# Performance work log

Hardware: AMD Instinct MI355X
Metric: run time of the kernel (lower is better)

Reference implementation:

```python
import jax, jax.numpy as jnp
import numpy as np

# Dimensions (LRA BigBird base-ish config)
B, S, D = 4, 4096, 512
H, DH = 8, 64          # num_heads, head_dim = qkv_dim // num_heads
M = 2048               # mlp_dim
BS = 64                # block_size
NB = S // BS           # number of blocks = 64
R = 3                  # num random blocks per row (BigBird default)
K = 8                  # max gathered key blocks per row: 3 window + 2 global + 3 random
SEED = 0               # connectivity_seed
LN_EPS = 1e-6


def _block_indices():
    """Static BigBird connectivity for interior query blocks (rows 1..NB-2).

    Each interior block attends to: window {i-1,i,i+1}, globals {0, NB-1},
    and R random blocks (seeded, disjoint from window/global). Rows where
    window overlaps globals have fewer unique blocks and are padded+masked.
    """
    rng = np.random.RandomState(SEED)
    idx = np.zeros((NB - 2, K), np.int32)
    msk = np.zeros((NB - 2, K), bool)
    for row, i in enumerate(range(1, NB - 1)):
        fixed = sorted({0, NB - 1, i - 1, i, i + 1})
        allowed = [b for b in range(NB) if b not in fixed]
        rand = rng.choice(allowed, size=R, replace=False).tolist()
        blocks = fixed + rand
        idx[row, :len(blocks)] = blocks
        msk[row, :len(blocks)] = True
    return jnp.asarray(idx), jnp.asarray(msk)

IDX, KMASK = _block_indices()  # [NB-2, K] int32 / bool
NEG = -1e9


def _ln(x, scale, bias):
    mu = jnp.mean(x, axis=-1, keepdims=True)
    var = jnp.mean(jnp.square(x - mu), axis=-1, keepdims=True)
    return (x - mu) * jax.lax.rsqrt(var + LN_EPS) * scale + bias


def setup_inputs() -> dict:
    key = jax.random.key(0)
    ks = jax.random.split(key, 7)

    def xav(k, shape, fan_in, fan_out):
        lim = float(np.sqrt(6.0 / (fan_in + fan_out)))
        return jax.random.uniform(k, shape, jnp.float32, -lim, lim)

    return {
        "inputs": jax.random.normal(ks[0], (B, S, D), jnp.float32),
        "ln1_scale": jnp.ones((D,), jnp.float32),
        "ln1_bias": jnp.zeros((D,), jnp.float32),
        "wq": xav(ks[1], (D, H, DH), D, DH),
        "wk": xav(ks[2], (D, H, DH), D, DH),
        "wv": xav(ks[3], (D, H, DH), D, DH),
        "wo": xav(ks[4], (H, DH, D), D, D),
        "ln2_scale": jnp.ones((D,), jnp.float32),
        "ln2_bias": jnp.zeros((D,), jnp.float32),
        "w1": xav(ks[5], (D, M), D, M),
        "b1": jnp.zeros((M,), jnp.float32),
        "w2": xav(ks[6], (M, D), M, D),
        "b2": jnp.zeros((D,), jnp.float32),
    }


def reference(inputs, ln1_scale, ln1_bias, wq, wk, wv, wo,
              ln2_scale, ln2_bias, w1, b1, w2, b2):
    x = _ln(inputs, ln1_scale, ln1_bias)
    scale = 1.0 / jnp.sqrt(jnp.asarray(DH, x.dtype))
    q = jnp.einsum("bsd,dhk->bshk", x, wq) * scale
    k = jnp.einsum("bsd,dhk->bshk", x, wk)
    v = jnp.einsum("bsd,dhk->bshk", x, wv)

    # block layout: [B, H, NB, BS, DH]
    qb = q.reshape(B, NB, BS, H, DH).transpose(0, 3, 1, 2, 4)
    kb = k.reshape(B, NB, BS, H, DH).transpose(0, 3, 1, 2, 4)
    vb = v.reshape(B, NB, BS, H, DH).transpose(0, 3, 1, 2, 4)

    # ---- interior query blocks: sparse (window + global + random) keys ----
    q_int = qb[:, :, 1:NB - 1]                       # [B,H,NB-2,BS,DH]
    k_sel = kb[:, :, IDX]                            # [B,H,NB-2,K,BS,DH]
    v_sel = vb[:, :, IDX]
    s = jnp.einsum("bhnqd,bhnkjd->bhnqkj", q_int, k_sel)
    s = jnp.where(KMASK[None, None, :, None, :, None], s, NEG)
    p = jax.nn.softmax(s.reshape(B, H, NB - 2, BS, K * BS), axis=-1)
    p = p.reshape(B, H, NB - 2, BS, K, BS)
    o_int = jnp.einsum("bhnqkj,bhnkjd->bhnqd", p, v_sel)

    # ---- global query blocks (first & last): full attention ----
    q_g = qb[:, :, jnp.array([0, NB - 1])]           # [B,H,2,BS,DH]
    kf = k.transpose(0, 2, 1, 3)                     # [B,H,S,DH]
    vf = v.transpose(0, 2, 1, 3)
    sg = jnp.einsum("bhgqd,bhtd->bhgqt", q_g, kf)
    pg = jax.nn.softmax(sg, axis=-1)
    o_g = jnp.einsum("bhgqt,bhtd->bhgqd", pg, vf)

    o = jnp.concatenate([o_g[:, :, :1], o_int, o_g[:, :, 1:]], axis=2)
    o = o.transpose(0, 2, 3, 1, 4).reshape(B, S, H, DH)
    attn = jnp.einsum("bshd,hde->bse", o, wo)        # output proj, no bias

    x = attn + inputs                                 # residual 1
    y = _ln(x, ln2_scale, ln2_bias)
    y = jax.nn.gelu(jnp.einsum("bsd,dm->bsm", y, w1) + b1)
    y = jnp.einsum("bsm,md->bsd", y, w2) + b2
    return x + y                                      # residual 2
```

## Files before the change

kernel.cpp:

```cpp
#include <hip/hip_runtime.h>
#include <cstdint>
#include <cstddef>

typedef __bf16 bf16;
typedef __bf16 bf16x8 __attribute__((ext_vector_type(8)));
typedef float  f32x4  __attribute__((ext_vector_type(4)));

#define DEVINL static __device__ __forceinline__

DEVINL void gl2lds16(const void* g, void* l) {
  __builtin_amdgcn_global_load_lds((__attribute__((address_space(1))) void*)g,
                                   (__attribute__((address_space(3))) void*)l,
                                   16, 0, 0);
}

DEVINL float loadf(const void* p, size_t i, int isf) {
  return isf ? ((const float*)p)[i] : (float)((const bf16*)p)[i];
}

struct TabArg { unsigned char idx[62][8]; unsigned char cnt[62]; };

struct HostMT {
  unsigned mt[624]; int mti;
  void seed(unsigned s) {
    mt[0] = s;
    for (int i = 1; i < 624; ++i) mt[i] = 1812433253u * (mt[i-1] ^ (mt[i-1] >> 30)) + (unsigned)i;
    mti = 624;
  }
  unsigned next() {
    if (mti == 624) {
      for (int i = 0; i < 624; ++i) {
        unsigned y = (mt[i] & 0x80000000u) | (mt[(i+1)%624] & 0x7fffffffu);
        unsigned v = mt[(i+397)%624] ^ (y >> 1);
        if (y & 1u) v ^= 0x9908b0dfu;
        mt[i] = v;
      }
      mti = 0;
    }
    unsigned y = mt[mti++];
    y ^= y >> 11; y ^= (y << 7) & 0x9d2c5680u; y ^= (y << 15) & 0xefc60000u; y ^= y >> 18;
    return y;
  }
  unsigned interval(unsigned mx) {
    if (mx == 0) return 0;
    unsigned mask = mx;
    mask |= mask>>1; mask |= mask>>2; mask |= mask>>4; mask |= mask>>8; mask |= mask>>16;
    unsigned v = next() & mask;
    while (v > mx) v = next() & mask;
    return v;
  }
};

static void build_tab(TabArg* t) {
  HostMT rng; rng.seed(0u);
  for (int row = 0; row < 62; ++row) {
    int i = row + 1;
    bool fix[64] = {};
    fix[0] = true; fix[63] = true; fix[i-1] = true; fix[i] = true; fix[i+1] = true;
    int fixed[5]; int nf = 0; int allowed[64]; int na = 0;
    for (int b = 0; b < 64; ++b) { if (fix[b]) fixed[nf++] = b; else allowed[na++] = b; }
    int perm[64];
    for (int j = 0; j < na; ++j) perm[j] = j;
    for (int j = na - 1; j > 0; --j) {
      unsigned kk = rng.interval((unsigned)j);
      int tmp = perm[j]; perm[j] = perm[kk]; perm[kk] = tmp;
    }
    int nb = 0;
    for (int j = 0; j < nf; ++j) t->idx[row][nb++] = (unsigned char)fixed[j];
    for (int j = 0; j < 3;  ++j) t->idx[row][nb++] = (unsigned char)allowed[perm[j]];
    t->cnt[row] = (unsigned char)nb;
    for (int j = nb; j < 8; ++j) t->idx[row][j] = 0;
  }
}

__global__ __launch_bounds__(256) void detect_kernel(const unsigned short* __restrict__ x,
                                                     int* __restrict__ flag) {
  __shared__ int cnt[256];
  int c = 0;
  for (int i = threadIdx.x; i < 8192; i += 256) {
    int e = (x[i] >> 7) & 0xFF;
    if (e >= 0xC6) c++;
  }
  cnt[threadIdx.x] = c;
  __syncthreads();
  for (int s = 128; s > 0; s >>= 1) {
    if (threadIdx.x < s) cnt[threadIdx.x] += cnt[threadIdx.x + s];
    __syncthreads();
  }
  if (threadIdx.x == 0) *flag = (cnt[0] > 32) ? 1 : 0;
}

struct P6 { const void* s[6]; bf16* d[6]; int n[6]; };
__global__ __launch_bounds__(256) void cvt6_kernel(const int* __restrict__ flagp, P6 p) {
  int isf = *flagp;
  int which = blockIdx.x;
  const void* src = p.s[which];
  bf16* dst = p.d[which];
  int n = p.n[which];
  int i8 = threadIdx.x * 8;
  if (i8 >= n) return;
  bf16x8 o;
  if (isf) {
    const float* s = (const float*)src + i8;
    f32x4 a = *(const f32x4*)s;
    f32x4 b = *(const f32x4*)(s + 4);
#pragma unroll
    for (int j = 0; j < 4; ++j) { o[j] = (bf16)a[j]; o[4+j] = (bf16)b[j]; }
  } else {
    o = *(const bf16x8*)((const bf16*)src + i8);
  }
  *(bf16x8*)(dst + i8) = o;
}

__global__ __launch_bounds__(256) void transpose_any_kernel(const int* __restrict__ flagp,
                                                            const void* __restrict__ in,
                                                            bf16* __restrict__ out, int R, int C) {
  __shared__ __align__(16) bf16 sT[64 * 72];
  int isf = *flagp;
  int cb = C >> 6;
  int br = blockIdx.x / cb, bc = blockIdx.x % cb;
  int r0 = br * 64, c0 = bc * 64;
  int t = threadIdx.x;
#pragma unroll
  for (int p = 0; p < 2; ++p) {
    int cid = p * 256 + t;
    int r = cid >> 3, c = cid & 7;
    bf16x8 v;
    if (isf) {
      const float* s = (const float*)in + (size_t)(r0 + r) * C + c0 + c * 8;
      f32x4 a = *(const f32x4*)s;
      f32x4 b = *(const f32x4*)(s + 4);
#pragma unroll
      for (int j = 0; j < 4; ++j) { v[j] = (bf16)a[j]; v[4+j] = (bf16)b[j]; }
    } else {
      v = *(const bf16x8*)((const bf16*)in + (size_t)(r0 + r) * C + c0 + c * 8);
    }
    *(bf16x8*)&sT[r * 72 + c * 8] = v;
  }
  __syncthreads();
#pragma unroll
  for (int p = 0; p < 2; ++p) {
    int cid = p * 256 + t;
    int oc = cid >> 3, rc = cid & 7;
    bf16x8 vv;
#pragma unroll
    for (int i = 0; i < 8; ++i) vv[i] = sT[(rc * 8 + i) * 72 + oc];
    *(bf16x8*)&out[(size_t)(c0 + oc) * R + r0 + rc * 8] = vv;
  }
}

__global__ __launch_bounds__(256) void ln_any_kernel(const int* __restrict__ flagp,
                                                     const void* __restrict__ x,
                                                     const bf16* __restrict__ sc,
                                                     const bf16* __restrict__ bi,
                                                     bf16* __restrict__ out) {
  int isf = *flagp;
  int row  = blockIdx.x * 4 + (threadIdx.x >> 6);
  int lane = threadIdx.x & 63;
  float f[8];
  if (isf) {
    const float* xf = (const float*)x + (size_t)row * 512 + lane * 8;
    f32x4 a = *(const f32x4*)xf;
    f32x4 b = *(const f32x4*)(xf + 4);
#pragma unroll
    for (int j = 0; j < 4; ++j) { f[j] = a[j]; f[4+j] = b[j]; }
  } else {
    bf16x8 v = ((const bf16x8*)((const bf16*)x + (size_t)row * 512))[lane];
#pragma unroll
    for (int j = 0; j < 8; ++j) f[j] = (float)v[j];
  }
  float s = 0.f, s2 = 0.f;
#pragma unroll
  for (int i = 0; i < 8; ++i) { s += f[i]; s2 += f[i]*f[i]; }
#pragma unroll
  for (int o = 32; o > 0; o >>= 1) { s += __shfl_xor(s, o, 64); s2 += __shfl_xor(s2, o, 64); }
  float mu  = s  * (1.f/512.f);
  float var = s2 * (1.f/512.f) - mu*mu;
  float rs  = rsqrtf(fmaxf(var, 0.f) + 1e-6f);
  bf16x8 sv = ((const bf16x8*)sc)[lane];
  bf16x8 bv = ((const bf16x8*)bi)[lane];
  bf16x8 o8;
#pragma unroll
  for (int i = 0; i < 8; ++i) o8[i] = (bf16)((f[i]-mu)*rs*(float)sv[i] + (float)bv[i]);
  ((bf16x8*)(out + (size_t)row * 512))[lane] = o8;
}

__global__ __launch_bounds__(256) void ln_bf16_kernel(const bf16* __restrict__ x,
                                                      const bf16* __restrict__ sc,
                                                      const bf16* __restrict__ bi,
                                                      bf16* __restrict__ out) {
  int row  = blockIdx.x * 4 + (threadIdx.x >> 6);
  int lane = threadIdx.x & 63;
  bf16x8 v = ((const bf16x8*)(x + (size_t)row * 512))[lane];
  float f[8], s = 0.f, s2 = 0.f;
#pragma unroll
  for (int i = 0; i < 8; ++i) { f[i] = (float)v[i]; s += f[i]; s2 += f[i]*f[i]; }
#pragma unroll
  for (int o = 32; o > 0; o >>= 1) { s += __shfl_xor(s, o, 64); s2 += __shfl_xor(s2, o, 64); }
  float mu  = s  * (1.f/512.f);
  float var = s2 * (1.f/512.f) - mu*mu;
  float rs  = rsqrtf(fmaxf(var, 0.f) + 1e-6f);
  bf16x8 sv = ((const bf16x8*)sc)[lane];
  bf16x8 bv = ((const bf16x8*)bi)[lane];
  bf16x8 o8;
#pragma unroll
  for (int i = 0; i < 8; ++i) o8[i] = (bf16)((f[i]-mu)*rs*(float)sv[i] + (float)bv[i]);
  ((bf16x8*)(out + (size_t)row * 512))[lane] = o8;
}

__global__ __launch_bounds__(256) void transpose_v_kernel(const bf16* __restrict__ v,
                                                          bf16* __restrict__ vT) {
  __shared__ __align__(16) bf16 sT[64 * 72];
  int st = blockIdx.x & 63;
  int h  = (blockIdx.x >> 6) & 7;
  int b  = blockIdx.x >> 9;
  int s0 = st * 64;
  int t  = threadIdx.x;
  const size_t ibase = ((size_t)b * 4096) * 512 + h * 64;
#pragma unroll
  for (int p = 0; p < 2; ++p) {
    int cid = p * 256 + t;
    int r = cid >> 3, c = cid & 7;
    *(bf16x8*)&sT[r * 72 + c * 8] = *(const bf16x8*)&v[ibase + (size_t)(s0 + r) * 512 + c * 8];
  }
  __syncthreads();
  const size_t obase = ((size_t)(b * 8 + h) * 64) * 4096;
#pragma unroll
  for (int p = 0; p < 2; ++p) {
    int cid = p * 256 + t;
    int dh = cid >> 3, scn = cid & 7;
    bf16x8 vv;
#pragma unroll
    for (int i = 0; i < 8; ++i) vv[i] = sT[(scn * 8 + i) * 72 + dh];
    *(bf16x8*)&vT[obase + (size_t)dh * 4096 + s0 + scn * 8] = vv;
  }
}

__global__ __launch_bounds__(256) void gemm_kernel(const bf16* __restrict__ A,
                                                   const bf16* __restrict__ BT,
                                                   int M, int N, int K,
                                                   int epi,
                                                   const bf16* __restrict__ bias,
                                                   const void* __restrict__ resid,
                                                   void* __restrict__ gout,
                                                   bf16* __restrict__ out2,
                                                   bf16* __restrict__ out3,
                                                   size_t gout_off,
                                                   const int* __restrict__ flagp) {
  __shared__ __align__(16) bf16 As[128 * 32];
  __shared__ __align__(16) bf16 Bs[128 * 32];
  const int t = threadIdx.x;
  const int w = t >> 6, l = t & 63, quad = l >> 4, l15 = l & 15;
  const int wm = w >> 1, wn = w & 1;
  const int m0 = blockIdx.y * 128, n0 = blockIdx.x * 128;
  const int isf = (epi == 1 || epi == 3) ? *flagp : 0;
  f32x4 acc[4][4] = {};
  const int nk = K >> 5;
  for (int kt = 0; kt < nk; ++kt) {
    __syncthreads();
#pragma unroll
    for (int p = 0; p < 2; ++p) {
      int cid = p * 256 + t;
      int r = cid >> 2, c = cid & 3;
      int sc_ = c ^ (r & 3);
      gl2lds16(A  + (size_t)(m0 + r) * K + kt * 32 + sc_ * 8, (char*)As + cid * 16);
      gl2lds16(BT + (size_t)(n0 + r) * K + kt * 32 + sc_ * 8, (char*)Bs + cid * 16);
    }
    __syncthreads();
    bf16x8 af[4], bfr[4];
#pragma unroll
    for (int mt = 0; mt < 4; ++mt) {
      int r = wm * 64 + mt * 16 + l15;
      af[mt] = *(const bf16x8*)&As[r * 32 + ((quad ^ (r & 3)) << 3)];
    }
#pragma unroll
    for (int nt = 0; nt < 4; ++nt) {
      int r = wn * 64 + nt * 16 + l15;
      bfr[nt] = *(const bf16x8*)&Bs[r * 32 + ((quad ^ (r & 3)) << 3)];
    }
#pragma unroll
    for (int mt = 0; mt < 4; ++mt)
#pragma unroll
      for (int nt = 0; nt < 4; ++nt)
        acc[mt][nt] = __builtin_amdgcn_mfma_f32_16x16x32_bf16(af[mt], bfr[nt], acc[mt][nt], 0, 0, 0);
  }
#pragma unroll
  for (int mt = 0; mt < 4; ++mt) {
    int rowb = m0 + wm * 64 + mt * 16 + quad * 4;
#pragma unroll
    for (int nt = 0; nt < 4; ++nt) {
      int col = n0 + wn * 64 + nt * 16 + l15;
#pragma unroll
      for (int r = 0; r < 4; ++r) {
        int row = rowb + r;
        float vacc = acc[mt][nt][r];
        size_t oidx = (size_t)row * N + col;
        if (epi == 5) {
          int which = col >> 9, c2 = col & 511;
          bf16 ov = (bf16)(which == 0 ? vacc * 0.125f : vacc);
          bf16* dst = which == 0 ? (bf16*)gout : (which == 1 ? out2 : out3);
          dst[(size_t)row * 512 + c2] = ov;
        } else if (epi == 1) {
          ((bf16*)gout)[oidx] = (bf16)(vacc + loadf(resid, oidx, isf));
        } else if (epi == 2) {
          float xv = vacc + (float)bias[col];
          float g = 0.5f * xv * (1.f + tanhf(0.7978845608028654f * (xv + 0.044715f * xv * xv * xv)));
          ((bf16*)gout)[oidx] = (bf16)g;
        } else {
          float v = vacc + (float)bias[col] + (float)((const bf16*)resid)[oidx];
          if (isf) ((float*)gout)[gout_off + oidx] = v;
          else     ((bf16*)gout)[gout_off + oidx] = (bf16)v;
        }
      }
    }
  }
}

__global__ __launch_bounds__(256) void attn_kernel(TabArg targ,
                                                   const bf16* __restrict__ q,
                                                   const bf16* __restrict__ k,
                                                   const bf16* __restrict__ vT,
                                                   bf16* __restrict__ o,
                                                   float* __restrict__ part,
                                                   int mode) {
  __shared__ __align__(16) bf16 sQ[64 * 64];
  __shared__ __align__(16) bf16 sK[64 * 64];
  __shared__ __align__(16) bf16 sV[64 * 64];
  __shared__ __align__(16) bf16 sP[64 * 64];

  const int t = threadIdx.x;
  const int w = t >> 6, l = t & 63, quad = l >> 4, l15 = l & 15;
  int n, bh, chunk = 0, niter;
  if (mode == 0) {
    n = 1 + (int)(blockIdx.x % 62);
    bh = blockIdx.x / 62;
    niter = (int)targ.cnt[n - 1];
  } else {
    chunk = blockIdx.x & 7;
    int g = (blockIdx.x >> 3) & 1;
    bh = blockIdx.x >> 4;
    n = g ? 63 : 0;
    niter = 8;
  }
  const int b = bh >> 3, h = bh & 7;
  const size_t bh_qk = ((size_t)b * 4096) * 512 + h * 64;
  const size_t bh_v  = ((size_t)(b * 8 + h) * 64) * 4096;

#pragma unroll
  for (int p = 0; p < 2; ++p) {
    int cid = p * 256 + t;
    int r = cid >> 3, c = cid & 7;
    int sc_ = c ^ (r & 7);
    gl2lds16(q + bh_qk + (size_t)(n * 64 + r) * 512 + sc_ * 8, (char*)sQ + cid * 16);
  }

  float m_r[4], l_r[4];
#pragma unroll
  for (int r = 0; r < 4; ++r) { m_r[r] = -1e30f; l_r[r] = 0.f; }
  f32x4 accO[4] = {};

  for (int it = 0; it < niter; ++it) {
    int kb = (mode == 0) ? (int)targ.idx[n - 1][it] : chunk * 8 + it;
    __syncthreads();
#pragma unroll
    for (int p = 0; p < 2; ++p) {
      int cid = p * 256 + t;
      int r = cid >> 3, c = cid & 7;
      int sc_ = c ^ (r & 7);
      gl2lds16(k  + bh_qk + (size_t)(kb * 64 + r) * 512 + sc_ * 8, (char*)sK + cid * 16);
      gl2lds16(vT + bh_v  + (size_t)r * 4096 + kb * 64 + sc_ * 8,  (char*)sV + cid * 16);
    }
    __syncthreads();

    f32x4 accS[4] = {};
#pragma unroll
    for (int ks = 0; ks < 2; ++ks) {
      int rQ = w * 16 + l15;
      int cc = ks * 4 + quad;
      bf16x8 afr = *(const bf16x8*)&sQ[rQ * 64 + ((cc ^ (rQ & 7)) << 3)];
#pragma unroll
      for (int j = 0; j < 4; ++j) {
        int rK = j * 16 + l15;
        bf16x8 bfr = *(const bf16x8*)&sK[rK * 64 + ((cc ^ (rK & 7)) << 3)];
        accS[j] = __builtin_amdgcn_mfma_f32_16x16x32_bf16(afr, bfr, accS[j], 0, 0, 0);
      }
    }

    float al[4];
#pragma unroll
    for (int r = 0; r < 4; ++r) {
      float mx = fmaxf(fmaxf(accS[0][r], accS[1][r]), fmaxf(accS[2][r], accS[3][r]));
#pragma unroll
      for (int off = 1; off < 16; off <<= 1) mx = fmaxf(mx, __shfl_xor(mx, off, 64));
      float mnew = fmaxf(m_r[r], mx);
      al[r] = __expf(m_r[r] - mnew);
      m_r[r] = mnew;
      int rowp = w * 16 + quad * 4 + r;
      float ps = 0.f;
#pragma unroll
      for (int j = 0; j < 4; ++j) {
        float pv = __expf(accS[j][r] - mnew);
        ps += pv;
        int col = j * 16 + l15;
        sP[rowp * 64 + (((col >> 3) ^ (rowp & 7)) << 3) + (col & 7)] = (bf16)pv;
      }
#pragma unroll
      for (int off = 1; off < 16; off <<= 1) ps += __shfl_xor(ps, off, 64);
      l_r[r] = l_r[r] * al[r] + ps;
    }

#pragma unroll
    for (int dt = 0; dt < 4; ++dt)
#pragma unroll
      for (int r = 0; r < 4; ++r) accO[dt][r] *= al[r];
#pragma unroll
    for (int ks = 0; ks < 2; ++ks) {
      int rP = w * 16 + l15;
      int cc = ks * 4 + quad;
      bf16x8 afr = *(const bf16x8*)&sP[rP * 64 + ((cc ^ (rP & 7)) << 3)];
#pragma unroll
      for (int dt = 0; dt < 4; ++dt) {
        int rV = dt * 16 + l15;
        bf16x8 bfr = *(const bf16x8*)&sV[rV * 64 + ((cc ^ (rV & 7)) << 3)];
        accO[dt] = __builtin_amdgcn_mfma_f32_16x16x32_bf16(afr, bfr, accO[dt], 0, 0, 0);
      }
    }
  }

  if (mode == 0) {
#pragma unroll
    for (int r = 0; r < 4; ++r) {
      int qr = w * 16 + quad * 4 + r;
      float linv = 1.f / fmaxf(l_r[r], 1e-30f);
      int srow = n * 64 + qr;
#pragma unroll
      for (int dt = 0; dt < 4; ++dt)
        o[bh_qk + (size_t)srow * 512 + dt * 16 + l15] = (bf16)(accO[dt][r] * linv);
    }
  } else {
    float* pb = part + (size_t)blockIdx.x * (4096 + 128);
#pragma unroll
    for (int r = 0; r < 4; ++r) {
      int row = w * 16 + quad * 4 + r;
#pragma unroll
      for (int dt = 0; dt < 4; ++dt)
        pb[row * 64 + dt * 16 + l15] = accO[dt][r];
      if (l15 == 0) { pb[4096 + row] = m_r[r]; pb[4160 + row] = l_r[r]; }
    }
  }
}

__global__ __launch_bounds__(256) void merge_kernel(const float* __restrict__ part,
                                                    bf16* __restrict__ o) {
  const int SP = 4096 + 128;
  int g = blockIdx.x & 1, bh = blockIdx.x >> 1;
  int b = bh >> 3, h = bh & 7, n = g ? 63 : 0;
  int t = threadIdx.x;
  int row = t >> 2, st = t & 3;
  size_t pb0 = (size_t)(bh * 16 + g * 8) * SP;
  float mc[8], lc[8], M = -1e30f;
#pragma unroll
  for (int c = 0; c < 8; ++c) {
    mc[c] = part[pb0 + (size_t)c * SP + 4096 + row];
    lc[c] = part[pb0 + (size_t)c * SP + 4160 + row];
    M = fmaxf(M, mc[c]);
  }
  float L = 0.f;
  float sc[8];
#pragma unroll
  for (int c = 0; c < 8; ++c) { sc[c] = __expf(mc[c] - M); L += lc[c] * sc[c]; }
  float inv = 1.f / fmaxf(L, 1e-30f);
  f32x4 acc[4] = {};
#pragma unroll
  for (int c = 0; c < 8; ++c) {
    const float* Op = part + pb0 + (size_t)c * SP + row * 64 + st * 16;
    float s = sc[c];
#pragma unroll
    for (int i = 0; i < 4; ++i) {
      f32x4 v = *(const f32x4*)(Op + i * 4);
#pragma unroll
      for (int j = 0; j < 4; ++j) acc[i][j] += v[j] * s;
    }
  }
  size_t obase = ((size_t)b * 4096 + n * 64 + row) * 512 + h * 64 + st * 16;
#pragma unroll
  for (int i = 0; i < 4; ++i)
#pragma unroll
    for (int j = 0; j < 4; ++j)
      o[obase + i * 4 + j] = (bf16)(acc[i][j] * inv);
}

extern "C" void kernel_launch(void* const* d_in, const int* in_sizes, int n_in,
                              void* d_out, int out_size, void* d_ws, size_t ws_size,
                              hipStream_t stream) {
  (void)in_sizes; (void)n_in; (void)out_size;
  const void* inputs = d_in[0];
  const void* ln1s = d_in[1];
  const void* ln1b = d_in[2];
  const void* wq   = d_in[3];
  const void* wk   = d_in[4];
  const void* wv   = d_in[5];
  const void* wo   = d_in[6];
  const void* ln2s = d_in[7];
  const void* ln2b = d_in[8];
  const void* w1   = d_in[9];
  const void* b1   = d_in[10];
  const void* w2   = d_in[11];
  const void* b2   = d_in[12];

  TabArg tab;
  build_tab(&tab);

  char* ws = (char*)d_ws;
  size_t off = 0;
  auto alloc = [&](size_t bytes) -> char* {
    char* p = ws + off; off += (bytes + 255) & ~(size_t)255; return p;
  };
  int*  flag   = (int*)alloc(256);
  bf16* ln1s_c = (bf16*)alloc(512 * 2);
  bf16* ln1b_c = (bf16*)alloc(512 * 2);
  bf16* ln2s_c = (bf16*)alloc(512 * 2);
  bf16* ln2b_c = (bf16*)alloc(512 * 2);
  bf16* b1_c   = (bf16*)alloc(2048 * 2);
  bf16* b2_c   = (bf16*)alloc(512 * 2);
  bf16* wqkvT  = (bf16*)alloc(1536ull * 512 * 2);
  bf16* woT    = (bf16*)alloc(512ull * 512 * 2);
  bf16* w1T    = (bf16*)alloc(512ull * 2048 * 2);
  bf16* w2T    = (bf16*)alloc(2048ull * 512 * 2);
  const size_t SZ = 16384ull * 512 * 2;
  bf16* regA = (bf16*)alloc(SZ);
  bf16* regB = (bf16*)alloc(SZ);
  bf16* regC = (bf16*)alloc(SZ);
  bf16* regD = (bf16*)alloc(SZ);
  size_t base_need = off;
  const size_t H1_BYTES = 16384ull * 2048 * 2;
  bool full_ffn = (ws_size >= base_need + H1_BYTES + 256);
  bf16* h1f = full_ffn ? (bf16*)alloc(H1_BYTES) : nullptr;

  bf16* xln  = regA;
  bf16* qb   = regB;
  bf16* kb   = regC;
  bf16* vb   = regD;
  bf16* vTb  = regA;
  bf16* obuf = regD;
  bf16* xbuf = regA;
  bf16* yln  = regB;
  bf16* h1c  = regC;
  float* part = (float*)d_out;

  detect_kernel<<<1, 256, 0, stream>>>((const unsigned short*)inputs, flag);

  P6 p6;
  p6.s[0]=ln1s; p6.s[1]=ln1b; p6.s[2]=ln2s; p6.s[3]=ln2b; p6.s[4]=b1; p6.s[5]=b2;
  p6.d[0]=ln1s_c; p6.d[1]=ln1b_c; p6.d[2]=ln2s_c; p6.d[3]=ln2b_c; p6.d[4]=b1_c; p6.d[5]=b2_c;
  p6.n[0]=512; p6.n[1]=512; p6.n[2]=512; p6.n[3]=512; p6.n[4]=2048; p6.n[5]=512;
  cvt6_kernel<<<6, 256, 0, stream>>>(flag, p6);

  transpose_any_kernel<<<64,  256, 0, stream>>>(flag, wq, wqkvT,               512, 512);
  transpose_any_kernel<<<64,  256, 0, stream>>>(flag, wk, wqkvT + 512ull*512,  512, 512);
  transpose_any_kernel<<<64,  256, 0, stream>>>(flag, wv, wqkvT + 1024ull*512, 512, 512);
  transpose_any_kernel<<<64,  256, 0, stream>>>(flag, wo, woT, 512, 512);
  transpose_any_kernel<<<256, 256, 0, stream>>>(flag, w1, w1T, 512, 2048);
  transpose_any_kernel<<<256, 256, 0, stream>>>(flag, w2, w2T, 2048, 512);

  ln_any_kernel<<<4096, 256, 0, stream>>>(flag, inputs, ln1s_c, ln1b_c, xln);

  gemm_kernel<<<dim3(12, 128), 256, 0, stream>>>(xln, wqkvT, 16384, 1536, 512, 5,
                                                 nullptr, nullptr, qb, kb, vb, 0, flag);

  transpose_v_kernel<<<2048, 256, 0, stream>>>(vb, vTb);

  attn_kernel<<<1984, 256, 0, stream>>>(tab, qb, kb, vTb, obuf, part, 0);
  attn_kernel<<<512,  256, 0, stream>>>(tab, qb, kb, vTb, obuf, part, 1);
  merge_kernel<<<64,  256, 0, stream>>>(part, obuf);

  gemm_kernel<<<dim3(4, 128), 256, 0, stream>>>(obuf, woT, 16384, 512, 512, 1,
                                                nullptr, inputs, xbuf, nullptr, nullptr, 0, flag);

  ln_bf16_kernel<<<4096, 256, 0, stream>>>(xbuf, ln2s_c, ln2b_c, yln);

  if (full_ffn) {
    gemm_kernel<<<dim3(16, 128), 256, 0, stream>>>(yln, w1T, 16384, 2048, 512, 2,
                                                   b1_c, nullptr, h1f, nullptr, nullptr, 0, flag);
    gemm_kernel<<<dim3(4, 128), 256, 0, stream>>>(h1f, w2T, 16384, 512, 2048, 3,
                                                  b2_c, xbuf, d_out, nullptr, nullptr, 0, flag);
  } else {
    for (int c = 0; c < 4; ++c) {
      const bf16* yc = yln  + (size_t)c * 4096 * 512;
      const bf16* xc = xbuf + (size_t)c * 4096 * 512;
      size_t oo = (size_t)c * 4096 * 512;
      gemm_kernel<<<dim3(16, 32), 256, 0, stream>>>(yc, w1T, 4096, 2048, 512, 2,
                                                    b1_c, nullptr, h1c, nullptr, nullptr, 0, flag);
      gemm_kernel<<<dim3(4, 32), 256, 0, stream>>>(h1c, w2T, 4096, 512, 2048, 3,
                                                   b2_c, xc, d_out, nullptr, nullptr, oo, flag);
    }
  }
}
```

Measured before the change: 510.8 us.

## Deepen GEMM K-tile to 64, batch weight transposes, use exp-based GELU

The GEMM kernel now stages 64-wide K slices in LDS, with an 8-way XOR swizzle and two MFMA sub-steps per tile. This halves the number of barrier and load rounds per output tile. The six separate weight-transpose launches are merged into one launch that picks its weight matrix by block index, cutting launch overhead. The tanh-based GELU in the FFN epilogue is rewritten as x*sigmoid(2u) using __expf, which is algebraically the same and cheaper but slightly less precise. The larger LDS footprint (32KB per block) may reduce occupancy.

```diff
diff --git a/kernel.cpp b/kernel.cpp
--- a/kernel.cpp
+++ b/kernel.cpp
@@ -16,6 +16,12 @@
 
 DEVINL float loadf(const void* p, size_t i, int isf) {
   return isf ? ((const float*)p)[i] : (float)((const bf16*)p)[i];
+}
+
+DEVINL float gelu_fast(float x) {
+  float u = 0.7978845608028654f * (x + 0.044715f * x * x * x);
+  float s = 1.f / (1.f + __expf(-2.f * u));
+  return x * s;
 }
 
 struct TabArg { unsigned char idx[62][8]; unsigned char cnt[62]; };
@@ -112,13 +118,19 @@
   *(bf16x8*)(dst + i8) = o;
 }
 
-__global__ __launch_bounds__(256) void transpose_any_kernel(const int* __restrict__ flagp,
-                                                            const void* __restrict__ in,
-                                                            bf16* __restrict__ out, int R, int C) {
+struct W6 { const void* in[6]; bf16* out[6]; int R[6], C[6], start[6]; };
+__global__ __launch_bounds__(256) void transpose_w6_kernel(const int* __restrict__ flagp, W6 wz) {
   __shared__ __align__(16) bf16 sT[64 * 72];
   int isf = *flagp;
+  int which = 0;
+#pragma unroll
+  for (int i = 1; i < 6; ++i) if ((int)blockIdx.x >= wz.start[i]) which = i;
+  const void* in = wz.in[which];
+  bf16* out = wz.out[which];
+  int R = wz.R[which], C = wz.C[which];
+  int bid = blockIdx.x - wz.start[which];
   int cb = C >> 6;
-  int br = blockIdx.x / cb, bc = blockIdx.x % cb;
+  int br = bid / cb, bc = bid % cb;
   int r0 = br * 64, c0 = bc * 64;
   int t = threadIdx.x;
 #pragma unroll
@@ -247,42 +259,46 @@
                                                    bf16* __restrict__ out3,
                                                    size_t gout_off,
                                                    const int* __restrict__ flagp) {
-  __shared__ __align__(16) bf16 As[128 * 32];
-  __shared__ __align__(16) bf16 Bs[128 * 32];
+  __shared__ __align__(16) bf16 As[128 * 64];
+  __shared__ __align__(16) bf16 Bs[128 * 64];
   const int t = threadIdx.x;
   const int w = t >> 6, l = t & 63, quad = l >> 4, l15 = l & 15;
   const int wm = w >> 1, wn = w & 1;
   const int m0 = blockIdx.y * 128, n0 = blockIdx.x * 128;
   const int isf = (epi == 1 || epi == 3) ? *flagp : 0;
   f32x4 acc[4][4] = {};
-  const int nk = K >> 5;
+  const int nk = K >> 6;
   for (int kt = 0; kt < nk; ++kt) {
     __syncthreads();
 #pragma unroll
-    for (int p = 0; p < 2; ++p) {
+    for (int p = 0; p < 4; ++p) {
       int cid = p * 256 + t;
-      int r = cid >> 2, c = cid & 3;
-      int sc_ = c ^ (r & 3);
-      gl2lds16(A  + (size_t)(m0 + r) * K + kt * 32 + sc_ * 8, (char*)As + cid * 16);
-      gl2lds16(BT + (size_t)(n0 + r) * K + kt * 32 + sc_ * 8, (char*)Bs + cid * 16);
+      int r = cid >> 3, c = cid & 7;
+      int sc_ = c ^ (r & 7);
+      gl2lds16(A  + (size_t)(m0 + r) * K + kt * 64 + sc_ * 8, (char*)As + cid * 16);
+      gl2lds16(BT + (size_t)(n0 + r) * K + kt * 64 + sc_ * 8, (char*)Bs + cid * 16);
     }
     __syncthreads();
-    bf16x8 af[4], bfr[4];
-#pragma unroll
-    for (int mt = 0; mt < 4; ++mt) {
-      int r = wm * 64 + mt * 16 + l15;
-      af[mt] = *(const bf16x8*)&As[r * 32 + ((quad ^ (r & 3)) << 3)];
-    }
-#pragma unroll
-    for (int nt = 0; nt < 4; ++nt) {
-      int r = wn * 64 + nt * 16 + l15;
-      bfr[nt] = *(const bf16x8*)&Bs[r * 32 + ((quad ^ (r & 3)) << 3)];
-    }
-#pragma unroll
-    for (int mt = 0; mt < 4; ++mt)
-#pragma unroll
-      for (int nt = 0; nt < 4; ++nt)
-        acc[mt][nt] = __builtin_amdgcn_mfma_f32_16x16x32_bf16(af[mt], bfr[nt], acc[mt][nt], 0, 0, 0);
+#pragma unroll
+    for (int ks = 0; ks < 2; ++ks) {
+      bf16x8 af[4], bfr[4];
+      int cc = ks * 4 + quad;
+#pragma unroll
+      for (int mt = 0; mt < 4; ++mt) {
+        int r = wm * 64 + mt * 16 + l15;
+        af[mt] = *(const bf16x8*)&As[r * 64 + ((cc ^ (r & 7)) << 3)];
+      }
+#pragma unroll
+      for (int nt = 0; nt < 4; ++nt) {
+        int r = wn * 64 + nt * 16 + l15;
+        bfr[nt] = *(const bf16x8*)&Bs[r * 64 + ((cc ^ (r & 7)) << 3)];
+      }
+#pragma unroll
+      for (int mt = 0; mt < 4; ++mt)
+#pragma unroll
+        for (int nt = 0; nt < 4; ++nt)
+          acc[mt][nt] = __builtin_amdgcn_mfma_f32_16x16x32_bf16(af[mt], bfr[nt], acc[mt][nt], 0, 0, 0);
+    }
   }
 #pragma unroll
   for (int mt = 0; mt < 4; ++mt) {
@@ -303,9 +319,7 @@
         } else if (epi == 1) {
           ((bf16*)gout)[oidx] = (bf16)(vacc + loadf(resid, oidx, isf));
         } else if (epi == 2) {
-          float xv = vacc + (float)bias[col];
-          float g = 0.5f * xv * (1.f + tanhf(0.7978845608028654f * (xv + 0.044715f * xv * xv * xv)));
-          ((bf16*)gout)[oidx] = (bf16)g;
+          ((bf16*)gout)[oidx] = (bf16)gelu_fast(vacc + (float)bias[col]);
         } else {
           float v = vacc + (float)bias[col] + (float)((const bf16*)resid)[oidx];
           if (isf) ((float*)gout)[gout_off + oidx] = v;
@@ -556,12 +570,14 @@
   p6.n[0]=512; p6.n[1]=512; p6.n[2]=512; p6.n[3]=512; p6.n[4]=2048; p6.n[5]=512;
   cvt6_kernel<<<6, 256, 0, stream>>>(flag, p6);
 
-  transpose_any_kernel<<<64,  256, 0, stream>>>(flag, wq, wqkvT,               512, 512);
-  transpose_any_kernel<<<64,  256, 0, stream>>>(flag, wk, wqkvT + 512ull*512,  512, 512);
-  transpose_any_kernel<<<64,  256, 0, stream>>>(flag, wv, wqkvT + 1024ull*512, 512, 512);
-  transpose_any_kernel<<<64,  256, 0, stream>>>(flag, wo, woT, 512, 512);
-  transpose_any_kernel<<<256, 256, 0, stream>>>(flag, w1, w1T, 512, 2048);
-  transpose_any_kernel<<<256, 256, 0, stream>>>(flag, w2, w2T, 2048, 512);
+  W6 w6;
+  w6.in[0]=wq; w6.in[1]=wk; w6.in[2]=wv; w6.in[3]=wo; w6.in[4]=w1; w6.in[5]=w2;
+  w6.out[0]=wqkvT; w6.out[1]=wqkvT+512ull*512; w6.out[2]=wqkvT+1024ull*512;
+  w6.out[3]=woT; w6.out[4]=w1T; w6.out[5]=w2T;
+  w6.R[0]=512; w6.R[1]=512; w6.R[2]=512; w6.R[3]=512; w6.R[4]=512;  w6.R[5]=2048;
+  w6.C[0]=512; w6.C[1]=512; w6.C[2]=512; w6.C[3]=512; w6.C[4]=2048; w6.C[5]=512;
+  w6.start[0]=0; w6.start[1]=64; w6.start[2]=128; w6.start[3]=192; w6.start[4]=256; w6.start[5]=512;
+  transpose_w6_kernel<<<768, 256, 0, stream>>>(flag, w6);
 
   ln_any_kernel<<<4096, 256, 0, stream>>>(flag, inputs, ln1s_c, ln1b_c, xln);
 
```

Result: faster. 479.6 us (-6.1%).
